# Performance work log

Hardware: AMD Instinct MI355X
Metric: run time of the kernel (lower is better)

## Reference

```python
import jax, jax.numpy as jnp
import numpy as np

H = 32  # hidden size (fixed in source)
V = 95  # input_size == output_size == vocab of chars


def _init_param(key, shape, fan):
    bound = 1.0 / np.sqrt(fan)
    return jax.random.uniform(key, shape, dtype=jnp.float32, minval=-bound, maxval=bound)


def setup_inputs() -> dict:
    key = jax.random.key(0)
    ks = jax.random.split(key, 16)
    B, T = 2048, 256
    inp = {"x": jax.random.normal(ks[0], (B, T, V), dtype=jnp.float32)}
    in_sizes = [V, H, H]
    i = 1
    for l, isz in enumerate(in_sizes, start=1):
        inp[f"Wih{l}"] = _init_param(ks[i], (3 * H, isz), H); i += 1
        inp[f"Whh{l}"] = _init_param(ks[i], (3 * H, H), H); i += 1
        inp[f"bih{l}"] = _init_param(ks[i], (3 * H,), H); i += 1
        inp[f"bhh{l}"] = _init_param(ks[i], (3 * H,), H); i += 1
    inp["Wfc"] = _init_param(ks[13], (V, H), H)
    inp["bfc"] = _init_param(ks[14], (V,), H)
    return inp


def gru_layer(x, Wih, Whh, bih, bhh):
    # x: [B, T, I] -> hs: [B, T, H]; PyTorch GRU gate math, h0 = 0.
    B, T, _ = x.shape
    # Precompute input projections for all timesteps (batched GEMM).
    xp = jnp.einsum('bti,gi->btg', x, Wih) + bih          # [B, T, 3H]
    xr, xz, xn = jnp.split(xp, 3, axis=-1)                # each [B, T, H]
    xs = (jnp.swapaxes(xr, 0, 1), jnp.swapaxes(xz, 0, 1), jnp.swapaxes(xn, 0, 1))
    Whr, Whz, Whn = jnp.split(Whh, 3, axis=0)             # each [H, H]
    bhr, bhz, bhn = jnp.split(bhh, 3, axis=0)

    def step(h, t_in):
        txr, txz, txn = t_in
        r = jax.nn.sigmoid(txr + h @ Whr.T + bhr)
        z = jax.nn.sigmoid(txz + h @ Whz.T + bhz)
        n = jnp.tanh(txn + r * (h @ Whn.T + bhn))
        h_new = (1.0 - z) * n + z * h
        return h_new, h_new

    h0 = jnp.zeros((B, Whh.shape[1]), dtype=x.dtype)
    _, hs = jax.lax.scan(step, h0, xs)                    # hs: [T, B, H]
    return jnp.swapaxes(hs, 0, 1)                         # [B, T, H]


def reference(x, Wih1, Whh1, bih1, bhh1, Wih2, Whh2, bih2, bhh2,
              Wih3, Whh3, bih3, bhh3, Wfc, bfc):
    out = gru_layer(x, Wih1, Whh1, bih1, bhh1)
    out = gru_layer(out, Wih2, Whh2, bih2, bhh2)
    out = gru_layer(out, Wih3, Whh3, bih3, bhh3)
    return jnp.einsum('bth,oh->bto', out, Wfc) + bfc      # [B, T, V]
```

## Files before the change

### kernel.cpp

```cpp
#include <hip/hip_runtime.h>

#define TT 256
#define VV 95

__device__ __forceinline__ float fast_sigmoid(float v) {
    return __builtin_amdgcn_rcpf(1.0f + __expf(-v));
}
__device__ __forceinline__ float fast_tanh(float v) {
    return 1.0f - 2.0f * __builtin_amdgcn_rcpf(__expf(2.0f * v) + 1.0f);
}
__device__ __forceinline__ void wave_fence() {
    asm volatile("s_waitcnt lgkmcnt(0)" ::: "memory");
    __builtin_amdgcn_wave_barrier();
}
__device__ __forceinline__ void vm_wait0() {
    asm volatile("s_waitcnt vmcnt(0)" ::: "memory");
}
__device__ __forceinline__ void gld_lds4(const float* g, float* lds) {
    __builtin_amdgcn_global_load_lds(
        (const __attribute__((address_space(1))) void*)g,
        (__attribute__((address_space(3))) void*)lds,
        4, 0, 0);
}
__device__ __forceinline__ void stage760(const float* g, float* lds, int l) {
    #pragma unroll
    for (int i = 0; i < 11; ++i) gld_lds4(g + i * 64 + l, lds + i * 64);
    if (l < 56) gld_lds4(g + 704 + l, lds + 704);
}
__device__ __forceinline__ void stage8x32(const float* g, float* lds, int l) {
    if (l < 32) {
        #pragma unroll
        for (int r = 0; r < 8; ++r) gld_lds4(g + r * VV + l, lds + r * 32);
    }
}

__device__ __forceinline__ float dot16(const float* w, float4 a, float4 b, float4 c, float4 d) {
    float s = 0.0f;
    s = fmaf(w[0],  a.x, s); s = fmaf(w[1],  a.y, s); s = fmaf(w[2],  a.z, s); s = fmaf(w[3],  a.w, s);
    s = fmaf(w[4],  b.x, s); s = fmaf(w[5],  b.y, s); s = fmaf(w[6],  b.z, s); s = fmaf(w[7],  b.w, s);
    s = fmaf(w[8],  c.x, s); s = fmaf(w[9],  c.y, s); s = fmaf(w[10], c.z, s); s = fmaf(w[11], c.w, s);
    s = fmaf(w[12], d.x, s); s = fmaf(w[13], d.y, s); s = fmaf(w[14], d.z, s); s = fmaf(w[15], d.w, s);
    return s;
}

__global__ void __launch_bounds__(256) k0_xproj(
    const float* __restrict__ x, const float* __restrict__ Wih1,
    const float* __restrict__ bih1, float* __restrict__ out)
{
    __shared__ float xs[64 * 100];
    __shared__ float ws[96 * 100];
    const int tid = threadIdx.x;
    const size_t row0 = (size_t)blockIdx.x * 64;

    const float* xg = x + row0 * VV;
    for (int i = tid; i < 64 * VV; i += 256) {
        const int r = i / VV, c = i - r * VV;
        xs[r * 100 + c] = xg[i];
    }
    for (int i = tid; i < 96 * VV; i += 256) {
        const int g = i / VV, c = i - g * VV;
        ws[g * 100 + c] = Wih1[i];
    }
    for (int i = tid; i < 64 * 5; i += 256) xs[(i / 5) * 100 + 95 + (i % 5)] = 0.f;
    for (int i = tid; i < 96 * 5; i += 256) ws[(i / 5) * 100 + 95 + (i % 5)] = 0.f;

    const int cq = tid & 15, rq = tid >> 4;
    float acc[4][6];
    #pragma unroll
    for (int c = 0; c < 6; ++c) {
        const float bv = bih1[cq + 16 * c];
        acc[0][c] = bv; acc[1][c] = bv; acc[2][c] = bv; acc[3][c] = bv;
    }
    __syncthreads();

    const float* xp0 = xs + rq * 100;
    const float* wp0 = ws + cq * 100;
    #pragma unroll 4
    for (int k4 = 0; k4 < 24; ++k4) {
        const int k = k4 * 4;
        float4 xv0 = *(const float4*)(xp0 + k);
        float4 xv1 = *(const float4*)(xp0 + 1600 + k);
        float4 xv2 = *(const float4*)(xp0 + 3200 + k);
        float4 xv3 = *(const float4*)(xp0 + 4800 + k);
        #pragma unroll
        for (int c = 0; c < 6; ++c) {
            const float4 wv = *(const float4*)(wp0 + c * 1600 + k);
            acc[0][c] = fmaf(xv0.x, wv.x, acc[0][c]); acc[0][c] = fmaf(xv0.y, wv.y, acc[0][c]);
            acc[0][c] = fmaf(xv0.z, wv.z, acc[0][c]); acc[0][c] = fmaf(xv0.w, wv.w, acc[0][c]);
            acc[1][c] = fmaf(xv1.x, wv.x, acc[1][c]); acc[1][c] = fmaf(xv1.y, wv.y, acc[1][c]);
            acc[1][c] = fmaf(xv1.z, wv.z, acc[1][c]); acc[1][c] = fmaf(xv1.w, wv.w, acc[1][c]);
            acc[2][c] = fmaf(xv2.x, wv.x, acc[2][c]); acc[2][c] = fmaf(xv2.y, wv.y, acc[2][c]);
            acc[2][c] = fmaf(xv2.z, wv.z, acc[2][c]); acc[2][c] = fmaf(xv2.w, wv.w, acc[2][c]);
            acc[3][c] = fmaf(xv3.x, wv.x, acc[3][c]); acc[3][c] = fmaf(xv3.y, wv.y, acc[3][c]);
            acc[3][c] = fmaf(xv3.z, wv.z, acc[3][c]); acc[3][c] = fmaf(xv3.w, wv.w, acc[3][c]);
        }
    }
    #pragma unroll
    for (int r = 0; r < 4; ++r) {
        float* orow = out + (row0 + rq + 16 * r) * VV;
        #pragma unroll
        for (int c = 0; c < 6; ++c) {
            const int g = cq + 16 * c;
            if (g < VV) orow[g] = acc[r][c];
        }
    }
}

extern "C" __global__ void __launch_bounds__(256, 2) k1_l1(
    const float* __restrict__ x, const float* __restrict__ Wih1,
    const float* __restrict__ Whh1, const float* __restrict__ bih1,
    const float* __restrict__ bhh1, float* __restrict__ out)
{
    __shared__ __align__(16) float xpb[4][2][768];
    __shared__ __align__(16) float xb [4][2][768];
    __shared__ __align__(16) float hb[4][32];

    const int tid = threadIdx.x;
    const int w = tid >> 6, l = tid & 63, p = l >> 5, j = l & 31;

    float ur[16], uz[16], un[16];
    #pragma unroll
    for (int c = 0; c < 16; ++c) {
        ur[c] = Whh1[j * 32 + 16 * p + c];
        uz[c] = Whh1[(32 + j) * 32 + 16 * p + c];
        un[c] = Whh1[(64 + j) * 32 + 16 * p + c];
    }
    const float bhr = bhh1[j], bhz = bhh1[32 + j], bhn = bhh1[64 + j];
    const float wa = Wih1[95 * VV + l];
    const float wb = (l < 31) ? Wih1[95 * VV + 64 + l] : 0.f;
    const float bn95 = bih1[95];

    const size_t b = (size_t)blockIdx.x * 4 + w;
    const float* xrow = x + b * (size_t)(TT * VV);
    float* orow = out + b * (size_t)(TT * VV);

    if (p == 0) hb[w][j] = 0.f;
    float hj = 0.f;

    stage760(orow, &xpb[w][0][0], l);
    stage760(xrow, &xb[w][0][0], l);
    wave_fence();

    for (int t = 0; t < TT; ++t) {
        const int tc = t & 7;
        const int cb = (t >> 3) & 1;
        if (tc == 0) {
            vm_wait0();
            if (t + 8 < TT) {
                stage760(orow + (t + 8) * VV, &xpb[w][cb ^ 1][0], l);
                stage760(xrow + (t + 8) * VV, &xb[w][cb ^ 1][0], l);
            }
        }
        const float* xpc = &xpb[w][cb][tc * VV];
        const float* xc  = &xb [w][cb][tc * VV];
        const float xr  = xpc[j];
        const float xz  = xpc[32 + j];
        const float xn  = (j < 31) ? xpc[64 + j] : 0.f;
        const float xav = xc[l];
        const float xbv = (l < 31) ? xc[64 + l] : 0.f;

        float v = fmaf(wa, xav, wb * xbv);
        v += __shfl_xor(v, 1);  v += __shfl_xor(v, 2);  v += __shfl_xor(v, 4);
        v += __shfl_xor(v, 8);  v += __shfl_xor(v, 16); v += __shfl_xor(v, 32);

        const float4* hv = (const float4*)(&hb[w][16 * p]);
        const float4 h0 = hv[0], h1v = hv[1], h2v = hv[2], h3v = hv[3];
        float hr = dot16(ur, h0, h1v, h2v, h3v);
        float hz = dot16(uz, h0, h1v, h2v, h3v);
        float hn = dot16(un, h0, h1v, h2v, h3v);
        hr += __shfl_xor(hr, 32);
        hz += __shfl_xor(hz, 32);
        hn += __shfl_xor(hn, 32);

        const float xnf = (j == 31) ? (v + bn95) : xn;
        const float r = fast_sigmoid(xr + hr + bhr);
        const float z = fast_sigmoid(xz + hz + bhz);
        const float n = fast_tanh(xnf + r * (hn + bhn));
        hj = (1.0f - z) * n + z * hj;

        asm volatile("" ::: "memory");
        if (p == 0) { hb[w][j] = hj; orow[t * VV + j] = hj; }
        wave_fence();
    }
}

extern "C" __global__ void __launch_bounds__(256, 2) k23_layer(
    const float* __restrict__ Wih, const float* __restrict__ Whh,
    const float* __restrict__ bih, const float* __restrict__ bhh,
    float* __restrict__ out, int in_col)
{
    __shared__ __align__(16) float ib[4][2][256];
    __shared__ __align__(16) float hb[4][32];

    const int tid = threadIdx.x;
    const int w = tid >> 6, l = tid & 63, p = l >> 5, j = l & 31;

    float vr[16], vz[16], vn[16], ur[16], uz[16], un[16];
    #pragma unroll
    for (int c = 0; c < 16; ++c) {
        vr[c] = Wih[j * 32 + 16 * p + c];
        vz[c] = Wih[(32 + j) * 32 + 16 * p + c];
        vn[c] = Wih[(64 + j) * 32 + 16 * p + c];
        ur[c] = Whh[j * 32 + 16 * p + c];
        uz[c] = Whh[(32 + j) * 32 + 16 * p + c];
        un[c] = Whh[(64 + j) * 32 + 16 * p + c];
    }
    const float br  = bih[j] + bhh[j];
    const float bz  = bih[32 + j] + bhh[32 + j];
    const float bni = bih[64 + j], bnh = bhh[64 + j];

    const size_t b = (size_t)blockIdx.x * 4 + w;
    float* orow = out + b * (size_t)(TT * VV);

    if (p == 0) hb[w][j] = 0.f;
    float hj = 0.f;

    stage8x32(orow + in_col, &ib[w][0][0], l);
    wave_fence();

    for (int t = 0; t < TT; ++t) {
        const int tc = t & 7;
        const int cb = (t >> 3) & 1;
        if (tc == 0) {
            vm_wait0();
            if (t + 8 < TT)
                stage8x32(orow + (t + 8) * VV + in_col, &ib[w][cb ^ 1][0], l);
        }
        const float4* iv = (const float4*)(&ib[w][cb][tc * 32 + 16 * p]);
        const float4 a0 = iv[0], a1 = iv[1], a2 = iv[2], a3 = iv[3];
        const float4* hv = (const float4*)(&hb[w][16 * p]);
        const float4 h0 = hv[0], h1v = hv[1], h2v = hv[2], h3v = hv[3];

        float ar = dot16(vr, a0, a1, a2, a3);
        float az = dot16(vz, a0, a1, a2, a3);
        float an = dot16(vn, a0, a1, a2, a3);
        float hr = dot16(ur, h0, h1v, h2v, h3v);
        float hz = dot16(uz, h0, h1v, h2v, h3v);
        float hn = dot16(un, h0, h1v, h2v, h3v);

        float s1 = ar + hr; s1 += __shfl_xor(s1, 32);
        float s2 = az + hz; s2 += __shfl_xor(s2, 32);
        an += __shfl_xor(an, 32);
        hn += __shfl_xor(hn, 32);

        const float r = fast_sigmoid(s1 + br);
        const float z = fast_sigmoid(s2 + bz);
        const float n = fast_tanh(an + bni + r * (hn + bnh));
        hj = (1.0f - z) * n + z * hj;

        asm volatile("" ::: "memory");
        if (p == 0) { hb[w][j] = hj; orow[t * VV + 32 + j] = hj; }
        wave_fence();
    }
}

__global__ void __launch_bounds__(256) k4_fc(
    const float* __restrict__ Wfc, const float* __restrict__ bfc,
    float* __restrict__ out)
{
    __shared__ float hs[64 * 36];
    __shared__ float ws[96 * 36];
    const int tid = threadIdx.x;
    const size_t row0 = (size_t)blockIdx.x * 64;

    for (int i = tid; i < 64 * 32; i += 256) {
        const int r = i >> 5, k = i & 31;
        hs[r * 36 + k] = out[(row0 + r) * VV + 32 + k];
    }
    for (int i = tid; i < 95 * 32; i += 256) {
        const int g = i >> 5, k = i & 31;
        ws[g * 36 + k] = Wfc[i];
    }
    for (int i = tid; i < 32; i += 256) ws[95 * 36 + i] = 0.f;
    const int cq = tid & 15, rq = tid >> 4;
    float acc[4][6];
    #pragma unroll
    for (int c = 0; c < 6; ++c) {
        const int g = cq + 16 * c;
        const float bv = (g < VV) ? bfc[g] : 0.f;
        acc[0][c] = bv; acc[1][c] = bv; acc[2][c] = bv; acc[3][c] = bv;
    }
    __syncthreads();

    #pragma unroll
    for (int k4 = 0; k4 < 8; ++k4) {
        const int k = k4 * 4;
        const float4 h0 = *(const float4*)(hs + (rq     ) * 36 + k);
        const float4 h1 = *(const float4*)(hs + (rq + 16) * 36 + k);
        const float4 h2 = *(const float4*)(hs + (rq + 32) * 36 + k);
        const float4 h3 = *(const float4*)(hs + (rq + 48) * 36 + k);
        #pragma unroll
        for (int c = 0; c < 6; ++c) {
            const float4 wv = *(const float4*)(ws + (cq + 16 * c) * 36 + k);
            acc[0][c] = fmaf(h0.x, wv.x, acc[0][c]); acc[0][c] = fmaf(h0.y, wv.y, acc[0][c]);
            acc[0][c] = fmaf(h0.z, wv.z, acc[0][c]); acc[0][c] = fmaf(h0.w, wv.w, acc[0][c]);
            acc[1][c] = fmaf(h1.x, wv.x, acc[1][c]); acc[1][c] = fmaf(h1.y, wv.y, acc[1][c]);
            acc[1][c] = fmaf(h1.z, wv.z, acc[1][c]); acc[1][c] = fmaf(h1.w, wv.w, acc[1][c]);
            acc[2][c] = fmaf(h2.x, wv.x, acc[2][c]); acc[2][c] = fmaf(h2.y, wv.y, acc[2][c]);
            acc[2][c] = fmaf(h2.z, wv.z, acc[2][c]); acc[2][c] = fmaf(h2.w, wv.w, acc[2][c]);
            acc[3][c] = fmaf(h3.x, wv.x, acc[3][c]); acc[3][c] = fmaf(h3.y, wv.y, acc[3][c]);
            acc[3][c] = fmaf(h3.z, wv.z, acc[3][c]); acc[3][c] = fmaf(h3.w, wv.w, acc[3][c]);
        }
    }
    #pragma unroll
    for (int r = 0; r < 4; ++r) {
        float* orow = out + (row0 + rq + 16 * r) * VV;
        #pragma unroll
        for (int c = 0; c < 6; ++c) {
            const int g = cq + 16 * c;
            if (g < VV) orow[g] = acc[r][c];
        }
    }
}

extern "C" void kernel_launch(void* const* d_in, const int* in_sizes, int n_in,
                              void* d_out, int out_size, void* d_ws, size_t ws_size,
                              hipStream_t stream) {
    const float* x    = (const float*)d_in[0];
    const float* Wih1 = (const float*)d_in[1];
    const float* Whh1 = (const float*)d_in[2];
    const float* bih1 = (const float*)d_in[3];
    const float* bhh1 = (const float*)d_in[4];
    const float* Wih2 = (const float*)d_in[5];
    const float* Whh2 = (const float*)d_in[6];
    const float* bih2 = (const float*)d_in[7];
    const float* bhh2 = (const float*)d_in[8];
    const float* Wih3 = (const float*)d_in[9];
    const float* Whh3 = (const float*)d_in[10];
    const float* bih3 = (const float*)d_in[11];
    const float* bhh3 = (const float*)d_in[12];
    const float* Wfc  = (const float*)d_in[13];
    const float* bfc  = (const float*)d_in[14];
    float* out = (float*)d_out;

    hipLaunchKernelGGL(k0_xproj,  dim3(8192), dim3(256), 0, stream, x, Wih1, bih1, out);
    hipLaunchKernelGGL(k1_l1,     dim3(512),  dim3(256), 0, stream, x, Wih1, Whh1, bih1, bhh1, out);
    hipLaunchKernelGGL(k23_layer, dim3(512),  dim3(256), 0, stream, Wih2, Whh2, bih2, bhh2, out, 0);
    hipLaunchKernelGGL(k23_layer, dim3(512),  dim3(256), 0, stream, Wih3, Whh3, bih3, bhh3, out, 32);
    hipLaunchKernelGGL(k4_fc,     dim3(8192), dim3(256), 0, stream, Wfc, bfc, out);
}
```

Baseline: 996.8 us.

## Broadcast hidden state via readlane, drop LDS round-trip in recurrent GRU kernels

The recurrent kernels for all three layers now keep a full 32-wide weight row per lane and broadcast the hidden state (and the layer input) to every lane with readlane. This replaces the LDS write/read and the wave fence on each timestep. Lanes 32-63 compute the z gate while lanes 0-31 compute r and n, exchanging results with one cross-half shuffle. Inputs are prefetched four steps ahead in registers instead of through LDS staging. Layer 1 gets its 95th input-projection column from a new workspace buffer, and layer 3 writes to columns 0-31 so the FC kernel reads from there. The cost is higher register pressure (up to 128 weight floats per lane) and a long serial chain of scalar readlanes.

```diff
diff --git a/kernel.cpp b/kernel.cpp
--- a/kernel.cpp
+++ b/kernel.cpp
@@ -9,6 +9,13 @@
 __device__ __forceinline__ float fast_tanh(float v) {
     return 1.0f - 2.0f * __builtin_amdgcn_rcpf(__expf(2.0f * v) + 1.0f);
 }
+__device__ __forceinline__ float RLf(float v, int lane) {
+    return __int_as_float(__builtin_amdgcn_readlane(__float_as_int(v), lane));
+}
+__device__ __forceinline__ float partner32(float x) {
+    return __shfl_xor(x, 32);
+}
+
 __device__ __forceinline__ void wave_fence() {
     asm volatile("s_waitcnt lgkmcnt(0)" ::: "memory");
     __builtin_amdgcn_wave_barrier();
@@ -27,13 +34,6 @@
     for (int i = 0; i < 11; ++i) gld_lds4(g + i * 64 + l, lds + i * 64);
     if (l < 56) gld_lds4(g + 704 + l, lds + 704);
 }
-__device__ __forceinline__ void stage8x32(const float* g, float* lds, int l) {
-    if (l < 32) {
-        #pragma unroll
-        for (int r = 0; r < 8; ++r) gld_lds4(g + r * VV + l, lds + r * 32);
-    }
-}
-
 __device__ __forceinline__ float dot16(const float* w, float4 a, float4 b, float4 c, float4 d) {
     float s = 0.0f;
     s = fmaf(w[0],  a.x, s); s = fmaf(w[1],  a.y, s); s = fmaf(w[2],  a.z, s); s = fmaf(w[3],  a.w, s);
@@ -45,7 +45,8 @@
 
 __global__ void __launch_bounds__(256) k0_xproj(
     const float* __restrict__ x, const float* __restrict__ Wih1,
-    const float* __restrict__ bih1, float* __restrict__ out)
+    const float* __restrict__ bih1, float* __restrict__ out,
+    float* __restrict__ ws95, int use_ws)
 {
     __shared__ float xs[64 * 100];
     __shared__ float ws[96 * 100];
@@ -102,11 +103,75 @@
         for (int c = 0; c < 6; ++c) {
             const int g = cq + 16 * c;
             if (g < VV) orow[g] = acc[r][c];
+            else if (use_ws) ws95[row0 + rq + 16 * r] = acc[r][c];
         }
     }
 }
 
-extern "C" __global__ void __launch_bounds__(256, 2) k1_l1(
+#define L1S(tt, A, N, Wv) do {                                          \
+    float nA = 0.f, nN = 0.f, nW = 0.f;                                 \
+    if ((tt) + 4 < TT) {                                                \
+        nA = orow[((tt) + 4) * VV + l];                                 \
+        nN = orow[((tt) + 4) * VV + nidx];                              \
+        nW = wsrow[(tt) + 4];                                           \
+    }                                                                   \
+    float a0 = bA, a1 = 0.f, b0 = bB, b1 = 0.f;                         \
+    _Pragma("unroll")                                                   \
+    for (int k = 0; k < 32; k += 2) {                                   \
+        const float s0 = RLf(vh, k), s1 = RLf(vh, k + 1);               \
+        a0 = fmaf(wA[k], s0, a0);   a1 = fmaf(wA[k + 1], s1, a1);       \
+        b0 = fmaf(wB[k], s0, b0);   b1 = fmaf(wB[k + 1], s1, b1);       \
+    }                                                                   \
+    const float val = (A) + a0 + a1;                                    \
+    const float oA = partner32(val);                                    \
+    const float r_ = fast_sigmoid(val);                                 \
+    const float z_ = fast_sigmoid(oA);                                  \
+    const float xn_ = (j == 31) ? (Wv) : (N);                           \
+    const float n_ = fast_tanh(xn_ + r_ * (b0 + b1));                   \
+    hj = (1.f - z_) * n_ + z_ * hj;                                     \
+    vh = hj;                                                            \
+    if (l < 32) orow[(tt) * VV + j] = hj;                               \
+    (A) = nA; (N) = nN; (Wv) = nW;                                      \
+} while (0)
+
+extern "C" __global__ void __launch_bounds__(256) k1_sgpr(
+    const float* __restrict__ Whh1, const float* __restrict__ bhh1,
+    const float* __restrict__ ws95, float* __restrict__ out)
+{
+    const int tid = threadIdx.x;
+    const int w = tid >> 6, l = tid & 63, j = l & 31;
+    const bool hi = l >= 32;
+
+    float wA[32], wB[32];
+    const int rA = (hi ? 32 : 0) + j;
+    #pragma unroll
+    for (int k = 0; k < 32; ++k) {
+        wA[k] = Whh1[rA * 32 + k];
+        wB[k] = hi ? 0.f : Whh1[(64 + j) * 32 + k];
+    }
+    const float bA = bhh1[rA];
+    const float bB = bhh1[64 + j];
+
+    const size_t b = (size_t)blockIdx.x * 4 + w;
+    float* orow = out + b * (size_t)(TT * VV);
+    const float* wsrow = ws95 + b * TT;
+
+    float vh = 0.f, hj = 0.f;
+    const int nidx = 64 + (j < 31 ? j : 30);
+    float A0 = orow[0 * VV + l], N0 = orow[0 * VV + nidx], W0 = wsrow[0];
+    float A1 = orow[1 * VV + l], N1 = orow[1 * VV + nidx], W1 = wsrow[1];
+    float A2 = orow[2 * VV + l], N2 = orow[2 * VV + nidx], W2 = wsrow[2];
+    float A3 = orow[3 * VV + l], N3 = orow[3 * VV + nidx], W3 = wsrow[3];
+
+    for (int t = 0; t < TT; t += 4) {
+        L1S(t + 0, A0, N0, W0);
+        L1S(t + 1, A1, N1, W1);
+        L1S(t + 2, A2, N2, W2);
+        L1S(t + 3, A3, N3, W3);
+    }
+}
+
+extern "C" __global__ void __launch_bounds__(256, 2) k1_l1_fb(
     const float* __restrict__ x, const float* __restrict__ Wih1,
     const float* __restrict__ Whh1, const float* __restrict__ bih1,
     const float* __restrict__ bhh1, float* __restrict__ out)
@@ -184,73 +249,65 @@
     }
 }
 
-extern "C" __global__ void __launch_bounds__(256, 2) k23_layer(
+#define K23S(tt, VIN) do {                                              \
+    float nI = 0.f;                                                     \
+    if ((tt) + 4 < TT) nI = irow[((tt) + 4) * VV + j];                  \
+    float a0 = bA, a1 = 0.f, c0 = bN, c1 = 0.f;                         \
+    _Pragma("unroll")                                                   \
+    for (int k = 0; k < 32; k += 2) {                                   \
+        const float i0 = RLf(VIN, k),     h0 = RLf(vh, k);              \
+        const float i1 = RLf(VIN, k + 1), h1 = RLf(vh, k + 1);          \
+        a0 = fmaf(wI[k], i0, a0);      a0 = fmaf(wH[k], h0, a0);        \
+        a1 = fmaf(wI[k + 1], i1, a1);  a1 = fmaf(wH[k + 1], h1, a1);    \
+        c0 = fmaf(wNI[k], i0, c0);     c0 = fmaf(wNH[k], h0, c0);       \
+        c1 = fmaf(wNI[k + 1], i1, c1); c1 = fmaf(wNH[k + 1], h1, c1);   \
+    }                                                                   \
+    const float valA = a0 + a1, valC = c0 + c1;                         \
+    const float oA = partner32(valA);                                   \
+    const float oC = partner32(valC);                                   \
+    const float r_ = fast_sigmoid(valA);                                \
+    const float z_ = fast_sigmoid(oA);                                  \
+    const float n_ = fast_tanh(valC + r_ * oC);                         \
+    hj = (1.f - z_) * n_ + z_ * hj;                                     \
+    vh = hj;                                                            \
+    if (l < 32) orow[(tt) * VV + out_col + j] = hj;                     \
+    (VIN) = nI;                                                         \
+} while (0)
+
+extern "C" __global__ void __launch_bounds__(256) k23_sgpr(
     const float* __restrict__ Wih, const float* __restrict__ Whh,
     const float* __restrict__ bih, const float* __restrict__ bhh,
-    float* __restrict__ out, int in_col)
+    float* __restrict__ out, int in_col, int out_col)
 {
-    __shared__ __align__(16) float ib[4][2][256];
-    __shared__ __align__(16) float hb[4][32];
-
     const int tid = threadIdx.x;
-    const int w = tid >> 6, l = tid & 63, p = l >> 5, j = l & 31;
-
-    float vr[16], vz[16], vn[16], ur[16], uz[16], un[16];
-    #pragma unroll
-    for (int c = 0; c < 16; ++c) {
-        vr[c] = Wih[j * 32 + 16 * p + c];
-        vz[c] = Wih[(32 + j) * 32 + 16 * p + c];
-        vn[c] = Wih[(64 + j) * 32 + 16 * p + c];
-        ur[c] = Whh[j * 32 + 16 * p + c];
-        uz[c] = Whh[(32 + j) * 32 + 16 * p + c];
-        un[c] = Whh[(64 + j) * 32 + 16 * p + c];
-    }
-    const float br  = bih[j] + bhh[j];
-    const float bz  = bih[32 + j] + bhh[32 + j];
-    const float bni = bih[64 + j], bnh = bhh[64 + j];
+    const int w = tid >> 6, l = tid & 63, j = l & 31;
+    const bool hi = l >= 32;
+
+    float wI[32], wH[32], wNI[32], wNH[32];
+    const int rA = (hi ? 32 : 0) + j;
+    #pragma unroll
+    for (int k = 0; k < 32; ++k) {
+        wI[k]  = Wih[rA * 32 + k];
+        wH[k]  = Whh[rA * 32 + k];
+        wNI[k] = hi ? 0.f : Wih[(64 + j) * 32 + k];
+        wNH[k] = hi ? Whh[(64 + j) * 32 + k] : 0.f;
+    }
+    const float bA = bih[rA] + bhh[rA];
+    const float bN = hi ? bhh[64 + j] : bih[64 + j];
 
     const size_t b = (size_t)blockIdx.x * 4 + w;
     float* orow = out + b * (size_t)(TT * VV);
-
-    if (p == 0) hb[w][j] = 0.f;
-    float hj = 0.f;
-
-    stage8x32(orow + in_col, &ib[w][0][0], l);
-    wave_fence();
-
-    for (int t = 0; t < TT; ++t) {
-        const int tc = t & 7;
-        const int cb = (t >> 3) & 1;
-        if (tc == 0) {
-            vm_wait0();
-            if (t + 8 < TT)
-                stage8x32(orow + (t + 8) * VV + in_col, &ib[w][cb ^ 1][0], l);
-        }
-        const float4* iv = (const float4*)(&ib[w][cb][tc * 32 + 16 * p]);
-        const float4 a0 = iv[0], a1 = iv[1], a2 = iv[2], a3 = iv[3];
-        const float4* hv = (const float4*)(&hb[w][16 * p]);
-        const float4 h0 = hv[0], h1v = hv[1], h2v = hv[2], h3v = hv[3];
-
-        float ar = dot16(vr, a0, a1, a2, a3);
-        float az = dot16(vz, a0, a1, a2, a3);
-        float an = dot16(vn, a0, a1, a2, a3);
-        float hr = dot16(ur, h0, h1v, h2v, h3v);
-        float hz = dot16(uz, h0, h1v, h2v, h3v);
-        float hn = dot16(un, h0, h1v, h2v, h3v);
-
-        float s1 = ar + hr; s1 += __shfl_xor(s1, 32);
-        float s2 = az + hz; s2 += __shfl_xor(s2, 32);
-        an += __shfl_xor(an, 32);
-        hn += __shfl_xor(hn, 32);
-
-        const float r = fast_sigmoid(s1 + br);
-        const float z = fast_sigmoid(s2 + bz);
-        const float n = fast_tanh(an + bni + r * (hn + bnh));
-        hj = (1.0f - z) * n + z * hj;
-
-        asm volatile("" ::: "memory");
-        if (p == 0) { hb[w][j] = hj; orow[t * VV + 32 + j] = hj; }
-        wave_fence();
+    const float* irow = orow + in_col;
+
+    float vh = 0.f, hj = 0.f;
+    float I0 = irow[0 * VV + j], I1 = irow[1 * VV + j];
+    float I2 = irow[2 * VV + j], I3 = irow[3 * VV + j];
+
+    for (int t = 0; t < TT; t += 4) {
+        K23S(t + 0, I0);
+        K23S(t + 1, I1);
+        K23S(t + 2, I2);
+        K23S(t + 3, I3);
     }
 }
 
@@ -265,7 +322,7 @@
 
     for (int i = tid; i < 64 * 32; i += 256) {
         const int r = i >> 5, k = i & 31;
-        hs[r * 36 + k] = out[(row0 + r) * VV + 32 + k];
+        hs[r * 36 + k] = out[(row0 + r) * VV + k];
     }
     for (int i = tid; i < 95 * 32; i += 256) {
         const int g = i >> 5, k = i & 31;
@@ -332,10 +389,20 @@
     const float* Wfc  = (const float*)d_in[13];
     const float* bfc  = (const float*)d_in[14];
     float* out = (float*)d_out;
-
-    hipLaunchKernelGGL(k0_xproj,  dim3(8192), dim3(256), 0, stream, x, Wih1, bih1, out);
-    hipLaunchKernelGGL(k1_l1,     dim3(512),  dim3(256), 0, stream, x, Wih1, Whh1, bih1, bhh1, out);
-    hipLaunchKernelGGL(k23_layer, dim3(512),  dim3(256), 0, stream, Wih2, Whh2, bih2, bhh2, out, 0);
-    hipLaunchKernelGGL(k23_layer, dim3(512),  dim3(256), 0, stream, Wih3, Whh3, bih3, bhh3, out, 32);
-    hipLaunchKernelGGL(k4_fc,     dim3(8192), dim3(256), 0, stream, Wfc, bfc, out);
-}
+    float* ws95 = (float*)d_ws;
+
+    const int use_ws = (ws_size >= (size_t)2048 * 256 * 4) ? 1 : 0;
+
+    hipLaunchKernelGGL(k0_xproj, dim3(8192), dim3(256), 0, stream,
+                       x, Wih1, bih1, out, ws95, use_ws);
+    if (use_ws)
+        hipLaunchKernelGGL(k1_sgpr, dim3(512), dim3(256), 0, stream, Whh1, bhh1, ws95, out);
+    else
+        hipLaunchKernelGGL(k1_l1_fb, dim3(512), dim3(256), 0, stream,
+                           x, Wih1, Whh1, bih1, bhh1, out);
+    hipLaunchKernelGGL(k23_sgpr, dim3(512), dim3(256), 0, stream,
+                       Wih2, Whh2, bih2, bhh2, out, 0, 32);
+    hipLaunchKernelGGL(k23_sgpr, dim3(512), dim3(256), 0, stream,
+                       Wih3, Whh3, bih3, bhh3, out, 32, 0);
+    hipLaunchKernelGGL(k4_fc, dim3(8192), dim3(256), 0, stream, Wfc, bfc, out);
+}
```

New measurement: 1.085 ms. 8.8% more time.
